# Kernel optimization log

Hardware: AMD Instinct MI355X
Metric: run time of the kernel (lower is better)

The kernel has to match this reference:

```python
import jax, jax.numpy as jnp
import numpy as np

N = 50000
E = 800000
IN_C, HID_C, OUT_C = 128, 128, 64


def setup_inputs() -> dict:
    key = jax.random.key(0)
    k1, k2, k3, k4 = jax.random.split(key, 4)
    x = jax.random.normal(k1, (N, IN_C), dtype=jnp.float32)
    edge_index = jax.random.randint(k2, (2, E), 0, N, dtype=jnp.int32)
    # Glorot-ish init for the two linear layers (PyG GCNConv uses glorot)
    W1 = jax.random.normal(k3, (IN_C, HID_C), dtype=jnp.float32) / np.sqrt(IN_C)
    b1 = jnp.zeros((HID_C,), dtype=jnp.float32)
    W2 = jax.random.normal(k4, (HID_C, OUT_C), dtype=jnp.float32) / np.sqrt(HID_C)
    b2 = jnp.zeros((OUT_C,), dtype=jnp.float32)
    return {"x": x, "edge_index": edge_index, "W1": W1, "b1": b1, "W2": W2, "b2": b2}


def _gcn_norm(edge_index, num_nodes):
    # Add self-loops, then symmetric normalization deg^{-1/2}[row]*deg^{-1/2}[col]
    loop = jnp.arange(num_nodes, dtype=edge_index.dtype)
    row = jnp.concatenate([edge_index[0], loop])  # [E+N] source
    col = jnp.concatenate([edge_index[1], loop])  # [E+N] destination
    deg = jax.ops.segment_sum(jnp.ones_like(col, dtype=jnp.float32), col,
                              num_segments=num_nodes)
    deg_isqrt = jax.lax.rsqrt(deg)  # deg >= 1 due to self-loops
    norm = deg_isqrt[row] * deg_isqrt[col]  # [E+N]
    return row, col, norm


def _gcn_conv(x, row, col, norm, W, b, num_nodes):
    x = x @ W                                   # [N, C_out]
    msg = x[row] * norm[:, None]                # gather + scale, [E+N, C_out]
    out = jax.ops.segment_sum(msg, col, num_segments=num_nodes)  # scatter-add
    return out + b


def reference(x, edge_index, W1, b1, W2, b2):
    num_nodes = x.shape[0]
    row, col, norm = _gcn_norm(edge_index, num_nodes)
    h = _gcn_conv(x, row, col, norm, W1, b1, num_nodes)
    h = jax.nn.relu(h)
    out = _gcn_conv(h, row, col, norm, W2, b2, num_nodes)
    return out
```

## Files before the change

kernel.cpp:

```cpp
#include <hip/hip_runtime.h>


typedef float f32x4 __attribute__((ext_vector_type(4)));
typedef short bf16x8 __attribute__((ext_vector_type(8)));

#define EPB 4096

__device__ inline float bf2f(unsigned short u) {
    return __uint_as_float(((unsigned int)u) << 16);
}
__device__ inline unsigned short f2bf(float f) {
    unsigned int x = __float_as_uint(f);
    x = x + 0x7FFFu + ((x >> 16) & 1u);
    return (unsigned short)(x >> 16);
}
__device__ inline float4 cvt4(ushort4 u) {
    return make_float4(bf2f(u.x), bf2f(u.y), bf2f(u.z), bf2f(u.w));
}
__device__ inline void add4(float4& a, float4 v) {
    a.x += v.x; a.y += v.y; a.z += v.z; a.w += v.w;
}

__global__ __launch_bounds__(256) void k_rhist(const int* __restrict__ col,
                                               int* __restrict__ bbase,
                                               int* __restrict__ bucket_cnt,
                                               const float* __restrict__ W1,
                                               const float* __restrict__ W2,
                                               unsigned short* __restrict__ Wt1,
                                               unsigned short* __restrict__ Wt2,
                                               int e, int nbR, int nbB) {
    if ((int)blockIdx.x >= nbR) {
        int i = ((int)blockIdx.x - nbR) * 256 + threadIdx.x;
        if (i < 16384) {
            int k = i >> 7, nc = i & 127;
            Wt1[nc * 128 + k] = f2bf(W1[i]);
        } else if (i < 24576) {
            int i2 = i - 16384;
            int k = i2 >> 6, nc = i2 & 63;
            Wt2[nc * 128 + k] = f2bf(W2[i2]);
        }
        return;
    }
    __shared__ int h[256];
    int t = threadIdx.x;
    h[t] = 0;
    __syncthreads();
    int base = blockIdx.x * EPB;
#pragma unroll
    for (int i = 0; i < EPB / 256; ++i) {
        int idx = base + t + i * 256;
        if (idx < e) atomicAdd(&h[col[idx] >> 8], 1);
    }
    __syncthreads();
    if (t < nbB) bbase[t * nbR + blockIdx.x] = atomicAdd(&bucket_cnt[t], h[t]);
}

__global__ __launch_bounds__(256) void k_rscatter(const int* __restrict__ row,
                                                  const int* __restrict__ col,
                                                  const int* __restrict__ bucket_cnt,
                                                  const int* __restrict__ bbase,
                                                  unsigned int* __restrict__ tmp,
                                                  int e, int nbR, int nbB) {
    __shared__ int base[256];
    __shared__ int h[256];
    int t = threadIdx.x;
    int v = (t < nbB) ? bucket_cnt[t] : 0;
    base[t] = v;
    __syncthreads();
#pragma unroll
    for (int off = 1; off < 256; off <<= 1) {
        int u = (t >= off) ? base[t - off] : 0;
        __syncthreads();
        base[t] += u;
        __syncthreads();
    }
    int excl = base[t] - v;
    base[t] = excl + ((t < nbB) ? bbase[t * nbR + blockIdx.x] : 0);
    h[t] = 0;
    __syncthreads();
    int b0 = blockIdx.x * EPB;
#pragma unroll
    for (int i = 0; i < EPB / 256; ++i) {
        int idx = b0 + t + i * 256;
        if (idx < e) {
            int c = col[idx];
            int bin = c >> 8;
            int rk = atomicAdd(&h[bin], 1);
            tmp[base[bin] + rk] =
                ((unsigned int)(c & 255) << 16) | (unsigned int)row[idx];
        }
    }
}

__global__ __launch_bounds__(256) void k_bsort(const unsigned int* __restrict__ tmp,
                                               const int* __restrict__ bucket_cnt,
                                               int* __restrict__ indptr,
                                               float* __restrict__ dinv,
                                               unsigned short* __restrict__ srcidx,
                                               int n, int e, int nbB) {
    __shared__ int cnt[256];
    __shared__ int pre[256];
    int b = blockIdx.x;
    int t = threadIdx.x;

    int v = (t < nbB) ? bucket_cnt[t] : 0;
    pre[t] = v;
    __syncthreads();
#pragma unroll
    for (int off = 1; off < 256; off <<= 1) {
        int u = (t >= off) ? pre[t - off] : 0;
        __syncthreads();
        pre[t] += u;
        __syncthreads();
    }
    int beg = pre[b] - ((b < nbB) ? bucket_cnt[b] : 0);
    int end = pre[b];
    __syncthreads();

    cnt[t] = 0;
    __syncthreads();
    for (int i = beg + t; i < end; i += 256) atomicAdd(&cnt[tmp[i] >> 16], 1);
    __syncthreads();
    v = cnt[t];
    pre[t] = v;
    __syncthreads();
#pragma unroll
    for (int off = 1; off < 256; off <<= 1) {
        int u = (t >= off) ? pre[t - off] : 0;
        __syncthreads();
        pre[t] += u;
        __syncthreads();
    }
    int myexcl = pre[t] - v;
    int node = b * 256 + t;
    if (node < n) {
        indptr[node] = beg + myexcl;
        dinv[node] = rsqrtf((float)v + 1.0f);
    }
    if (b == nbB - 1 && t == 0) indptr[n] = e;
    __syncthreads();
    pre[t] = beg + myexcl;
    cnt[t] = 0;
    __syncthreads();
    for (int i = beg + t; i < end; i += 256) {
        unsigned int u = tmp[i];
        int cl = u >> 16;
        int rk = atomicAdd(&cnt[cl], 1);
        srcidx[pre[cl] + rk] = (unsigned short)(u & 0xFFFFu);
    }
}

__global__ __launch_bounds__(256, 2) void k_gemm1(const float* __restrict__ x,
                                                  const unsigned short* __restrict__ Wt,
                                                  const float* __restrict__ dinv,
                                                  unsigned short* __restrict__ hs, int n) {
    __shared__ unsigned short Xs[128 * 136];
    __shared__ unsigned short Ws[128 * 136];
    __shared__ float dinv_s[128];
    int t = threadIdx.x;
    int r0blk = blockIdx.x * 128;

#pragma unroll
    for (int i = 0; i < 8; ++i) {
        int c = t + i * 256;
        int nc = c >> 4;
        int k0 = (c & 15) * 8;
        bf16x8 v = *(const bf16x8*)&Wt[nc * 128 + k0];
        *(bf16x8*)&Ws[nc * 136 + k0] = v;
    }
#pragma unroll
    for (int i = 0; i < 16; ++i) {
        int c = t + i * 256;
        int r = c >> 5;
        int kq = c & 31;
        float4 v = make_float4(0.f, 0.f, 0.f, 0.f);
        int gr = r0blk + r;
        if (gr < n) v = ((const float4*)x)[gr * 32 + kq];
        ushort4 o;
        o.x = f2bf(v.x); o.y = f2bf(v.y); o.z = f2bf(v.z); o.w = f2bf(v.w);
        *(ushort4*)&Xs[r * 136 + kq * 4] = o;
    }
    if (t < 128) {
        int gr = r0blk + t;
        dinv_s[t] = (gr < n) ? dinv[gr] : 0.f;
    }
    __syncthreads();

    int lane = t & 63, wave = t >> 6;
    int lrow = lane & 15;
    int lk = (lane >> 4) * 8;

    f32x4 acc[2][8];
#pragma unroll
    for (int mi = 0; mi < 2; ++mi)
#pragma unroll
        for (int ni = 0; ni < 8; ++ni) acc[mi][ni] = (f32x4){0.f, 0.f, 0.f, 0.f};

#pragma unroll
    for (int ks = 0; ks < 4; ++ks) {
        int kk = ks * 32 + lk;
        bf16x8 a0 = *(bf16x8*)&Xs[(wave * 32 + lrow) * 136 + kk];
        bf16x8 a1 = *(bf16x8*)&Xs[(wave * 32 + 16 + lrow) * 136 + kk];
#pragma unroll
        for (int ni = 0; ni < 8; ++ni) {
            bf16x8 b = *(bf16x8*)&Ws[(ni * 16 + lrow) * 136 + kk];
            acc[0][ni] = __builtin_amdgcn_mfma_f32_16x16x32_bf16(a0, b, acc[0][ni], 0, 0, 0);
            acc[1][ni] = __builtin_amdgcn_mfma_f32_16x16x32_bf16(a1, b, acc[1][ni], 0, 0, 0);
        }
    }

    int rq = (lane >> 4) * 4;
#pragma unroll
    for (int mi = 0; mi < 2; ++mi)
#pragma unroll
        for (int r = 0; r < 4; ++r) {
            int lrw = wave * 32 + mi * 16 + rq + r;
            int grow = r0blk + lrw;
            if (grow < n) {
                float dv = dinv_s[lrw];
#pragma unroll
                for (int ni = 0; ni < 8; ++ni)
                    hs[grow * 128 + ni * 16 + lrow] = f2bf(acc[mi][ni][r] * dv);
            }
        }
}

__global__ __launch_bounds__(256) void k_gather1(const int* __restrict__ indptr,
                                                 const unsigned short* __restrict__ srcidx,
                                                 const unsigned short* __restrict__ hs,
                                                 const float* __restrict__ dinv,
                                                 const float* __restrict__ b1,
                                                 unsigned short* __restrict__ h1, int n) {
    int wid = (blockIdx.x * 256 + threadIdx.x) >> 6;
    if (wid >= n) return;
    int lane = threadIdx.x & 63;
    int half = lane >> 5;
    int hl = lane & 31;
    const ushort4* hv = (const ushort4*)hs;

    int beg = indptr[wid], end = indptr[wid + 1];
    int c0 = (end - beg + 1) >> 1;
    int j    = beg + half * c0;
    int jend = half ? end : (beg + c0);

    float4 a0 = make_float4(0.f, 0.f, 0.f, 0.f), a1 = a0, a2 = a0, a3 = a0;

    for (; j + 7 < jend; j += 8) {
        int s0 = srcidx[j],     s1 = srcidx[j + 1];
        int s2 = srcidx[j + 2], s3 = srcidx[j + 3];
        int s4 = srcidx[j + 4], s5 = srcidx[j + 5];
        int s6 = srcidx[j + 6], s7 = srcidx[j + 7];
        float4 v0 = cvt4(hv[s0 * 32 + hl]);
        float4 v1 = cvt4(hv[s1 * 32 + hl]);
        float4 v2 = cvt4(hv[s2 * 32 + hl]);
        float4 v3 = cvt4(hv[s3 * 32 + hl]);
        float4 v4 = cvt4(hv[s4 * 32 + hl]);
        float4 v5 = cvt4(hv[s5 * 32 + hl]);
        float4 v6 = cvt4(hv[s6 * 32 + hl]);
        float4 v7 = cvt4(hv[s7 * 32 + hl]);
        add4(a0, v0); add4(a1, v1); add4(a2, v2); add4(a3, v3);
        add4(a0, v4); add4(a1, v5); add4(a2, v6); add4(a3, v7);
    }
    if (j + 3 < jend) {
        int s0 = srcidx[j], s1 = srcidx[j + 1], s2 = srcidx[j + 2], s3 = srcidx[j + 3];
        add4(a0, cvt4(hv[s0 * 32 + hl]));
        add4(a1, cvt4(hv[s1 * 32 + hl]));
        add4(a2, cvt4(hv[s2 * 32 + hl]));
        add4(a3, cvt4(hv[s3 * 32 + hl]));
        j += 4;
    }
    for (; j < jend; ++j) add4(a0, cvt4(hv[srcidx[j] * 32 + hl]));

    if (half == 0) add4(a1, cvt4(hv[wid * 32 + hl]));

    float4 tsum;
    tsum.x = a0.x + a1.x + a2.x + a3.x;
    tsum.y = a0.y + a1.y + a2.y + a3.y;
    tsum.z = a0.z + a1.z + a2.z + a3.z;
    tsum.w = a0.w + a1.w + a2.w + a3.w;
    tsum.x += __shfl_xor(tsum.x, 32);
    tsum.y += __shfl_xor(tsum.y, 32);
    tsum.z += __shfl_xor(tsum.z, 32);
    tsum.w += __shfl_xor(tsum.w, 32);

    if (half == 0) {
        float d = dinv[wid];
        float4 bb = *(const float4*)&b1[hl * 4];
        ushort4 o;
        o.x = f2bf(fmaxf(tsum.x * d + bb.x, 0.f));
        o.y = f2bf(fmaxf(tsum.y * d + bb.y, 0.f));
        o.z = f2bf(fmaxf(tsum.z * d + bb.z, 0.f));
        o.w = f2bf(fmaxf(tsum.w * d + bb.w, 0.f));
        ((ushort4*)h1)[wid * 32 + hl] = o;
    }
}

__global__ __launch_bounds__(256, 3) void k_gemm2(const unsigned short* __restrict__ h1,
                                                  const unsigned short* __restrict__ Wt,
                                                  const float* __restrict__ dinv,
                                                  unsigned short* __restrict__ ps2, int n) {
    __shared__ unsigned short Xs[128 * 136];
    __shared__ unsigned short Ws[64 * 136];
    __shared__ float dinv_s[128];
    int t = threadIdx.x;
    int r0blk = blockIdx.x * 128;

#pragma unroll
    for (int i = 0; i < 4; ++i) {
        int c = t + i * 256;
        int nc = c >> 4;
        int k0 = (c & 15) * 8;
        bf16x8 v = *(const bf16x8*)&Wt[nc * 128 + k0];
        *(bf16x8*)&Ws[nc * 136 + k0] = v;
    }
#pragma unroll
    for (int i = 0; i < 8; ++i) {
        int c = t + i * 256;
        int r = c >> 4;
        int k0 = (c & 15) * 8;
        int gr = r0blk + r;
        bf16x8 v = (bf16x8)(short)0;
        if (gr < n) v = *(const bf16x8*)&h1[gr * 128 + k0];
        *(bf16x8*)&Xs[r * 136 + k0] = v;
    }
    if (t < 128) {
        int gr = r0blk + t;
        dinv_s[t] = (gr < n) ? dinv[gr] : 0.f;
    }
    __syncthreads();

    int lane = t & 63, wave = t >> 6;
    int lrow = lane & 15;
    int lk = (lane >> 4) * 8;

    f32x4 acc[2][4];
#pragma unroll
    for (int mi = 0; mi < 2; ++mi)
#pragma unroll
        for (int ni = 0; ni < 4; ++ni) acc[mi][ni] = (f32x4){0.f, 0.f, 0.f, 0.f};

#pragma unroll
    for (int ks = 0; ks < 4; ++ks) {
        int kk = ks * 32 + lk;
        bf16x8 a0 = *(bf16x8*)&Xs[(wave * 32 + lrow) * 136 + kk];
        bf16x8 a1 = *(bf16x8*)&Xs[(wave * 32 + 16 + lrow) * 136 + kk];
#pragma unroll
        for (int ni = 0; ni < 4; ++ni) {
            bf16x8 b = *(bf16x8*)&Ws[(ni * 16 + lrow) * 136 + kk];
            acc[0][ni] = __builtin_amdgcn_mfma_f32_16x16x32_bf16(a0, b, acc[0][ni], 0, 0, 0);
            acc[1][ni] = __builtin_amdgcn_mfma_f32_16x16x32_bf16(a1, b, acc[1][ni], 0, 0, 0);
        }
    }

    int rq = (lane >> 4) * 4;
#pragma unroll
    for (int mi = 0; mi < 2; ++mi)
#pragma unroll
        for (int r = 0; r < 4; ++r) {
            int lrw = wave * 32 + mi * 16 + rq + r;
            int grow = r0blk + lrw;
            if (grow < n) {
                float dv = dinv_s[lrw];
#pragma unroll
                for (int ni = 0; ni < 4; ++ni)
                    ps2[grow * 64 + ni * 16 + lrow] = f2bf(acc[mi][ni][r] * dv);
            }
        }
}

__global__ __launch_bounds__(256) void k_gather2(const int* __restrict__ indptr,
                                                 const unsigned short* __restrict__ srcidx,
                                                 const unsigned short* __restrict__ ps2,
                                                 const float* __restrict__ dinv,
                                                 const float* __restrict__ b2,
                                                 float* __restrict__ out, int n) {
    int wid = (blockIdx.x * 256 + threadIdx.x) >> 6;
    if (wid >= n) return;
    int lane = threadIdx.x & 63;
    int half = lane >> 5;
    int hl = lane & 31;
    const unsigned int* pv = (const unsigned int*)ps2;

    int beg = indptr[wid], end = indptr[wid + 1];
    int c0 = (end - beg + 1) >> 1;
    int j    = beg + half * c0;
    int jend = half ? end : (beg + c0);

    float2 a0 = make_float2(0.f, 0.f), a1 = a0, a2 = a0, a3 = a0;

    for (; j + 7 < jend; j += 8) {
        int s0 = srcidx[j],     s1 = srcidx[j + 1];
        int s2 = srcidx[j + 2], s3 = srcidx[j + 3];
        int s4 = srcidx[j + 4], s5 = srcidx[j + 5];
        int s6 = srcidx[j + 6], s7 = srcidx[j + 7];
        unsigned int u0 = pv[s0 * 32 + hl];
        unsigned int u1 = pv[s1 * 32 + hl];
        unsigned int u2 = pv[s2 * 32 + hl];
        unsigned int u3 = pv[s3 * 32 + hl];
        unsigned int u4 = pv[s4 * 32 + hl];
        unsigned int u5 = pv[s5 * 32 + hl];
        unsigned int u6 = pv[s6 * 32 + hl];
        unsigned int u7 = pv[s7 * 32 + hl];
        a0.x += bf2f((unsigned short)u0); a0.y += bf2f((unsigned short)(u0 >> 16));
        a1.x += bf2f((unsigned short)u1); a1.y += bf2f((unsigned short)(u1 >> 16));
        a2.x += bf2f((unsigned short)u2); a2.y += bf2f((unsigned short)(u2 >> 16));
        a3.x += bf2f((unsigned short)u3); a3.y += bf2f((unsigned short)(u3 >> 16));
        a0.x += bf2f((unsigned short)u4); a0.y += bf2f((unsigned short)(u4 >> 16));
        a1.x += bf2f((unsigned short)u5); a1.y += bf2f((unsigned short)(u5 >> 16));
        a2.x += bf2f((unsigned short)u6); a2.y += bf2f((unsigned short)(u6 >> 16));
        a3.x += bf2f((unsigned short)u7); a3.y += bf2f((unsigned short)(u7 >> 16));
    }
    if (j + 3 < jend) {
        int s0 = srcidx[j], s1 = srcidx[j + 1], s2 = srcidx[j + 2], s3 = srcidx[j + 3];
        unsigned int u0 = pv[s0 * 32 + hl];
        unsigned int u1 = pv[s1 * 32 + hl];
        unsigned int u2 = pv[s2 * 32 + hl];
        unsigned int u3 = pv[s3 * 32 + hl];
        a0.x += bf2f((unsigned short)u0); a0.y += bf2f((unsigned short)(u0 >> 16));
        a1.x += bf2f((unsigned short)u1); a1.y += bf2f((unsigned short)(u1 >> 16));
        a2.x += bf2f((unsigned short)u2); a2.y += bf2f((unsigned short)(u2 >> 16));
        a3.x += bf2f((unsigned short)u3); a3.y += bf2f((unsigned short)(u3 >> 16));
        j += 4;
    }
    for (; j < jend; ++j) {
        unsigned int u = pv[srcidx[j] * 32 + hl];
        a0.x += bf2f((unsigned short)u); a0.y += bf2f((unsigned short)(u >> 16));
    }

    if (half == 0) {
        unsigned int u = pv[wid * 32 + hl];
        a1.x += bf2f((unsigned short)u); a1.y += bf2f((unsigned short)(u >> 16));
    }

    float2 tsum;
    tsum.x = a0.x + a1.x + a2.x + a3.x;
    tsum.y = a0.y + a1.y + a2.y + a3.y;
    tsum.x += __shfl_xor(tsum.x, 32);
    tsum.y += __shfl_xor(tsum.y, 32);

    if (half == 0) {
        float d = dinv[wid];
        float2 bb = *(const float2*)&b2[hl * 2];
        float2 o;
        o.x = tsum.x * d + bb.x;
        o.y = tsum.y * d + bb.y;
        ((float2*)out)[wid * 32 + hl] = o;
    }
}

extern "C" void kernel_launch(void* const* d_in, const int* in_sizes, int n_in,
                              void* d_out, int out_size, void* d_ws, size_t ws_size,
                              hipStream_t stream) {
    const float* x  = (const float*)d_in[0];
    const int*   ei = (const int*)d_in[1];
    const float* W1 = (const float*)d_in[2];
    const float* b1 = (const float*)d_in[3];
    const float* W2 = (const float*)d_in[4];
    const float* b2 = (const float*)d_in[5];
    float* out = (float*)d_out;

    int n = in_sizes[0] / 128;
    int e = in_sizes[1] / 2;
    const int* row = ei;
    const int* col = ei + e;

    int nbR = (e + EPB - 1) / EPB;
    int nbB = (n + 255) / 256;
    int m   = nbB * nbR;

    int* iw = (int*)d_ws;
    size_t o = 0;
    int* bucket_cnt  = iw + o; o += 256;
    int* bbase       = iw + o; o += (size_t)m;           o = (o + 3) & ~(size_t)3;
    int* indptr      = iw + o; o += (size_t)(n + 1);     o = (o + 3) & ~(size_t)3;
    float* dinv      = (float*)(iw + o); o += (size_t)n; o = (o + 3) & ~(size_t)3;
    unsigned int* tmp = (unsigned int*)(iw + o); o += (size_t)e; o = (o + 3) & ~(size_t)3;
    unsigned short* srcidx = (unsigned short*)(iw + o); o += (size_t)(e / 2 + 2); o = (o + 3) & ~(size_t)3;
    unsigned short* Wt1 = (unsigned short*)(iw + o); o += 8192;
    unsigned short* Wt2 = (unsigned short*)(iw + o); o += 4096;
    unsigned short* hs  = (unsigned short*)(iw + o);
    unsigned short* h1  = hs + (size_t)n * 128;
    unsigned short* ps2 = hs;

    hipMemsetAsync(bucket_cnt, 0, 256 * sizeof(int), stream);
    k_rhist<<<nbR + 96, 256, 0, stream>>>(col, bbase, bucket_cnt, W1, W2, Wt1, Wt2, e, nbR, nbB);
    k_rscatter<<<nbR, 256, 0, stream>>>(row, col, bucket_cnt, bbase, tmp, e, nbR, nbB);
    k_bsort<<<nbB, 256, 0, stream>>>(tmp, bucket_cnt, indptr, dinv, srcidx, n, e, nbB);

    int nbg = (n + 127) / 128;
    k_gemm1<<<nbg, 256, 0, stream>>>(x, Wt1, dinv, hs, n);
    k_gather1<<<(n * 64 + 255) / 256, 256, 0, stream>>>(indptr, srcidx, hs, dinv, b1, h1, n);
    k_gemm2<<<nbg, 256, 0, stream>>>(h1, Wt2, dinv, ps2, n);
    k_gather2<<<(n * 64 + 255) / 256, 256, 0, stream>>>(indptr, srcidx, ps2, dinv, b2, out, n);
}
```

Measured before the change: 136.4 us.

## Fuse first GEMM into radix-scatter kernel and move source degree scaling into gather

Removes the dependency of the first GEMM on dinv by dropping the per-row source normalization from its epilogue and applying dinv[src] per edge inside gather1 instead. With that dependency gone, the GEMM blocks are launched in the same grid as the edge-scatter kernel, so both run concurrently and one launch is saved. The cost is an extra random dinv load per edge in gather1, plus the scatter blocks now carry the GEMM's large shared-memory footprint, which lowers their occupancy.

```diff
diff --git a/kernel.cpp b/kernel.cpp
--- a/kernel.cpp
+++ b/kernel.cpp
@@ -17,8 +17,8 @@
 __device__ inline float4 cvt4(ushort4 u) {
     return make_float4(bf2f(u.x), bf2f(u.y), bf2f(u.z), bf2f(u.w));
 }
-__device__ inline void add4(float4& a, float4 v) {
-    a.x += v.x; a.y += v.y; a.z += v.z; a.w += v.w;
+__device__ inline void fma4(float4& a, float4 v, float d) {
+    a.x += v.x * d; a.y += v.y * d; a.z += v.z * d; a.w += v.w * d;
 }
 
 __global__ __launch_bounds__(256) void k_rhist(const int* __restrict__ col,
@@ -55,41 +55,111 @@
     if (t < nbB) bbase[t * nbR + blockIdx.x] = atomicAdd(&bucket_cnt[t], h[t]);
 }
 
-__global__ __launch_bounds__(256) void k_rscatter(const int* __restrict__ row,
+__global__ __launch_bounds__(256, 2) void k_fused(const int* __restrict__ row,
                                                   const int* __restrict__ col,
                                                   const int* __restrict__ bucket_cnt,
                                                   const int* __restrict__ bbase,
                                                   unsigned int* __restrict__ tmp,
-                                                  int e, int nbR, int nbB) {
-    __shared__ int base[256];
-    __shared__ int h[256];
+                                                  const float* __restrict__ x,
+                                                  const unsigned short* __restrict__ Wt,
+                                                  unsigned short* __restrict__ hs,
+                                                  int e, int n, int nbR, int nbB) {
+    __shared__ int sbase[256];
+    __shared__ int sh[256];
+    __shared__ unsigned short Xs[128 * 136];
+    __shared__ unsigned short Ws[128 * 136];
     int t = threadIdx.x;
-    int v = (t < nbB) ? bucket_cnt[t] : 0;
-    base[t] = v;
-    __syncthreads();
-#pragma unroll
-    for (int off = 1; off < 256; off <<= 1) {
-        int u = (t >= off) ? base[t - off] : 0;
-        __syncthreads();
-        base[t] += u;
-        __syncthreads();
-    }
-    int excl = base[t] - v;
-    base[t] = excl + ((t < nbB) ? bbase[t * nbR + blockIdx.x] : 0);
-    h[t] = 0;
-    __syncthreads();
-    int b0 = blockIdx.x * EPB;
-#pragma unroll
-    for (int i = 0; i < EPB / 256; ++i) {
-        int idx = b0 + t + i * 256;
-        if (idx < e) {
-            int c = col[idx];
-            int bin = c >> 8;
-            int rk = atomicAdd(&h[bin], 1);
-            tmp[base[bin] + rk] =
-                ((unsigned int)(c & 255) << 16) | (unsigned int)row[idx];
-        }
-    }
+
+    if ((int)blockIdx.x < nbR) {
+        int v = (t < nbB) ? bucket_cnt[t] : 0;
+        sbase[t] = v;
+        __syncthreads();
+#pragma unroll
+        for (int off = 1; off < 256; off <<= 1) {
+            int u = (t >= off) ? sbase[t - off] : 0;
+            __syncthreads();
+            sbase[t] += u;
+            __syncthreads();
+        }
+        int excl = sbase[t] - v;
+        sbase[t] = excl + ((t < nbB) ? bbase[t * nbR + blockIdx.x] : 0);
+        sh[t] = 0;
+        __syncthreads();
+        int b0 = blockIdx.x * EPB;
+#pragma unroll
+        for (int i = 0; i < EPB / 256; ++i) {
+            int idx = b0 + t + i * 256;
+            if (idx < e) {
+                int c = col[idx];
+                int bin = c >> 8;
+                int rk = atomicAdd(&sh[bin], 1);
+                tmp[sbase[bin] + rk] =
+                    ((unsigned int)(c & 255) << 16) | (unsigned int)row[idx];
+            }
+        }
+        return;
+    }
+
+    int r0blk = ((int)blockIdx.x - nbR) * 128;
+
+#pragma unroll
+    for (int i = 0; i < 8; ++i) {
+        int c = t + i * 256;
+        int nc = c >> 4;
+        int k0 = (c & 15) * 8;
+        bf16x8 v = *(const bf16x8*)&Wt[nc * 128 + k0];
+        *(bf16x8*)&Ws[nc * 136 + k0] = v;
+    }
+#pragma unroll
+    for (int i = 0; i < 16; ++i) {
+        int c = t + i * 256;
+        int r = c >> 5;
+        int kq = c & 31;
+        float4 v = make_float4(0.f, 0.f, 0.f, 0.f);
+        int gr = r0blk + r;
+        if (gr < n) v = ((const float4*)x)[gr * 32 + kq];
+        ushort4 o;
+        o.x = f2bf(v.x); o.y = f2bf(v.y); o.z = f2bf(v.z); o.w = f2bf(v.w);
+        *(ushort4*)&Xs[r * 136 + kq * 4] = o;
+    }
+    __syncthreads();
+
+    int lane = t & 63, wave = t >> 6;
+    int lrow = lane & 15;
+    int lk = (lane >> 4) * 8;
+
+    f32x4 acc[2][8];
+#pragma unroll
+    for (int mi = 0; mi < 2; ++mi)
+#pragma unroll
+        for (int ni = 0; ni < 8; ++ni) acc[mi][ni] = (f32x4){0.f, 0.f, 0.f, 0.f};
+
+#pragma unroll
+    for (int ks = 0; ks < 4; ++ks) {
+        int kk = ks * 32 + lk;
+        bf16x8 a0 = *(bf16x8*)&Xs[(wave * 32 + lrow) * 136 + kk];
+        bf16x8 a1 = *(bf16x8*)&Xs[(wave * 32 + 16 + lrow) * 136 + kk];
+#pragma unroll
+        for (int ni = 0; ni < 8; ++ni) {
+            bf16x8 b = *(bf16x8*)&Ws[(ni * 16 + lrow) * 136 + kk];
+            acc[0][ni] = __builtin_amdgcn_mfma_f32_16x16x32_bf16(a0, b, acc[0][ni], 0, 0, 0);
+            acc[1][ni] = __builtin_amdgcn_mfma_f32_16x16x32_bf16(a1, b, acc[1][ni], 0, 0, 0);
+        }
+    }
+
+    int rq = (lane >> 4) * 4;
+#pragma unroll
+    for (int mi = 0; mi < 2; ++mi)
+#pragma unroll
+        for (int r = 0; r < 4; ++r) {
+            int lrw = wave * 32 + mi * 16 + rq + r;
+            int grow = r0blk + lrw;
+            if (grow < n) {
+#pragma unroll
+                for (int ni = 0; ni < 8; ++ni)
+                    hs[grow * 128 + ni * 16 + lrow] = f2bf(acc[mi][ni][r]);
+            }
+        }
 }
 
 __global__ __launch_bounds__(256) void k_bsort(const unsigned int* __restrict__ tmp,
@@ -148,81 +218,6 @@
         int rk = atomicAdd(&cnt[cl], 1);
         srcidx[pre[cl] + rk] = (unsigned short)(u & 0xFFFFu);
     }
-}
-
-__global__ __launch_bounds__(256, 2) void k_gemm1(const float* __restrict__ x,
-                                                  const unsigned short* __restrict__ Wt,
-                                                  const float* __restrict__ dinv,
-                                                  unsigned short* __restrict__ hs, int n) {
-    __shared__ unsigned short Xs[128 * 136];
-    __shared__ unsigned short Ws[128 * 136];
-    __shared__ float dinv_s[128];
-    int t = threadIdx.x;
-    int r0blk = blockIdx.x * 128;
-
-#pragma unroll
-    for (int i = 0; i < 8; ++i) {
-        int c = t + i * 256;
-        int nc = c >> 4;
-        int k0 = (c & 15) * 8;
-        bf16x8 v = *(const bf16x8*)&Wt[nc * 128 + k0];
-        *(bf16x8*)&Ws[nc * 136 + k0] = v;
-    }
-#pragma unroll
-    for (int i = 0; i < 16; ++i) {
-        int c = t + i * 256;
-        int r = c >> 5;
-        int kq = c & 31;
-        float4 v = make_float4(0.f, 0.f, 0.f, 0.f);
-        int gr = r0blk + r;
-        if (gr < n) v = ((const float4*)x)[gr * 32 + kq];
-        ushort4 o;
-        o.x = f2bf(v.x); o.y = f2bf(v.y); o.z = f2bf(v.z); o.w = f2bf(v.w);
-        *(ushort4*)&Xs[r * 136 + kq * 4] = o;
-    }
-    if (t < 128) {
-        int gr = r0blk + t;
-        dinv_s[t] = (gr < n) ? dinv[gr] : 0.f;
-    }
-    __syncthreads();
-
-    int lane = t & 63, wave = t >> 6;
-    int lrow = lane & 15;
-    int lk = (lane >> 4) * 8;
-
-    f32x4 acc[2][8];
-#pragma unroll
-    for (int mi = 0; mi < 2; ++mi)
-#pragma unroll
-        for (int ni = 0; ni < 8; ++ni) acc[mi][ni] = (f32x4){0.f, 0.f, 0.f, 0.f};
-
-#pragma unroll
-    for (int ks = 0; ks < 4; ++ks) {
-        int kk = ks * 32 + lk;
-        bf16x8 a0 = *(bf16x8*)&Xs[(wave * 32 + lrow) * 136 + kk];
-        bf16x8 a1 = *(bf16x8*)&Xs[(wave * 32 + 16 + lrow) * 136 + kk];
-#pragma unroll
-        for (int ni = 0; ni < 8; ++ni) {
-            bf16x8 b = *(bf16x8*)&Ws[(ni * 16 + lrow) * 136 + kk];
-            acc[0][ni] = __builtin_amdgcn_mfma_f32_16x16x32_bf16(a0, b, acc[0][ni], 0, 0, 0);
-            acc[1][ni] = __builtin_amdgcn_mfma_f32_16x16x32_bf16(a1, b, acc[1][ni], 0, 0, 0);
-        }
-    }
-
-    int rq = (lane >> 4) * 4;
-#pragma unroll
-    for (int mi = 0; mi < 2; ++mi)
-#pragma unroll
-        for (int r = 0; r < 4; ++r) {
-            int lrw = wave * 32 + mi * 16 + rq + r;
-            int grow = r0blk + lrw;
-            if (grow < n) {
-                float dv = dinv_s[lrw];
-#pragma unroll
-                for (int ni = 0; ni < 8; ++ni)
-                    hs[grow * 128 + ni * 16 + lrow] = f2bf(acc[mi][ni][r] * dv);
-            }
-        }
 }
 
 __global__ __launch_bounds__(256) void k_gather1(const int* __restrict__ indptr,
@@ -250,6 +245,8 @@
         int s2 = srcidx[j + 2], s3 = srcidx[j + 3];
         int s4 = srcidx[j + 4], s5 = srcidx[j + 5];
         int s6 = srcidx[j + 6], s7 = srcidx[j + 7];
+        float d0 = dinv[s0], d1 = dinv[s1], d2 = dinv[s2], d3 = dinv[s3];
+        float d4 = dinv[s4], d5 = dinv[s5], d6 = dinv[s6], d7 = dinv[s7];
         float4 v0 = cvt4(hv[s0 * 32 + hl]);
         float4 v1 = cvt4(hv[s1 * 32 + hl]);
         float4 v2 = cvt4(hv[s2 * 32 + hl]);
@@ -258,20 +255,24 @@
         float4 v5 = cvt4(hv[s5 * 32 + hl]);
         float4 v6 = cvt4(hv[s6 * 32 + hl]);
         float4 v7 = cvt4(hv[s7 * 32 + hl]);
-        add4(a0, v0); add4(a1, v1); add4(a2, v2); add4(a3, v3);
-        add4(a0, v4); add4(a1, v5); add4(a2, v6); add4(a3, v7);
+        fma4(a0, v0, d0); fma4(a1, v1, d1); fma4(a2, v2, d2); fma4(a3, v3, d3);
+        fma4(a0, v4, d4); fma4(a1, v5, d5); fma4(a2, v6, d6); fma4(a3, v7, d7);
     }
     if (j + 3 < jend) {
         int s0 = srcidx[j], s1 = srcidx[j + 1], s2 = srcidx[j + 2], s3 = srcidx[j + 3];
-        add4(a0, cvt4(hv[s0 * 32 + hl]));
-        add4(a1, cvt4(hv[s1 * 32 + hl]));
-        add4(a2, cvt4(hv[s2 * 32 + hl]));
-        add4(a3, cvt4(hv[s3 * 32 + hl]));
+        fma4(a0, cvt4(hv[s0 * 32 + hl]), dinv[s0]);
+        fma4(a1, cvt4(hv[s1 * 32 + hl]), dinv[s1]);
+        fma4(a2, cvt4(hv[s2 * 32 + hl]), dinv[s2]);
+        fma4(a3, cvt4(hv[s3 * 32 + hl]), dinv[s3]);
         j += 4;
     }
-    for (; j < jend; ++j) add4(a0, cvt4(hv[srcidx[j] * 32 + hl]));
-
-    if (half == 0) add4(a1, cvt4(hv[wid * 32 + hl]));
+    for (; j < jend; ++j) {
+        int s0 = srcidx[j];
+        fma4(a0, cvt4(hv[s0 * 32 + hl]), dinv[s0]);
+    }
+
+    float dw = dinv[wid];
+    if (half == 0) fma4(a1, cvt4(hv[wid * 32 + hl]), dw);
 
     float4 tsum;
     tsum.x = a0.x + a1.x + a2.x + a3.x;
@@ -284,13 +285,12 @@
     tsum.w += __shfl_xor(tsum.w, 32);
 
     if (half == 0) {
-        float d = dinv[wid];
         float4 bb = *(const float4*)&b1[hl * 4];
         ushort4 o;
-        o.x = f2bf(fmaxf(tsum.x * d + bb.x, 0.f));
-        o.y = f2bf(fmaxf(tsum.y * d + bb.y, 0.f));
-        o.z = f2bf(fmaxf(tsum.z * d + bb.z, 0.f));
-        o.w = f2bf(fmaxf(tsum.w * d + bb.w, 0.f));
+        o.x = f2bf(fmaxf(tsum.x * dw + bb.x, 0.f));
+        o.y = f2bf(fmaxf(tsum.y * dw + bb.y, 0.f));
+        o.z = f2bf(fmaxf(tsum.z * dw + bb.z, 0.f));
+        o.w = f2bf(fmaxf(tsum.w * dw + bb.w, 0.f));
         ((ushort4*)h1)[wid * 32 + hl] = o;
     }
 }
@@ -467,6 +467,7 @@
     int nbR = (e + EPB - 1) / EPB;
     int nbB = (n + 255) / 256;
     int m   = nbB * nbR;
+    int nbg = (n + 127) / 128;
 
     int* iw = (int*)d_ws;
     size_t o = 0;
@@ -484,11 +485,9 @@
 
     hipMemsetAsync(bucket_cnt, 0, 256 * sizeof(int), stream);
     k_rhist<<<nbR + 96, 256, 0, stream>>>(col, bbase, bucket_cnt, W1, W2, Wt1, Wt2, e, nbR, nbB);
-    k_rscatter<<<nbR, 256, 0, stream>>>(row, col, bucket_cnt, bbase, tmp, e, nbR, nbB);
+    k_fused<<<nbR + nbg, 256, 0, stream>>>(row, col, bucket_cnt, bbase, tmp, x, Wt1, hs, e, n, nbR, nbB);
     k_bsort<<<nbB, 256, 0, stream>>>(tmp, bucket_cnt, indptr, dinv, srcidx, n, e, nbB);
 
-    int nbg = (n + 127) / 128;
-    k_gemm1<<<nbg, 256, 0, stream>>>(x, Wt1, dinv, hs, n);
     k_gather1<<<(n * 64 + 255) / 256, 256, 0, stream>>>(indptr, srcidx, hs, dinv, b1, h1, n);
     k_gemm2<<<nbg, 256, 0, stream>>>(h1, Wt2, dinv, ps2, n);
     k_gather2<<<(n * 64 + 255) / 256, 256, 0, stream>>>(indptr, srcidx, ps2, dinv, b2, out, n);
```

After: 131.0 us (median of 2 runs). 1.04x faster.

## Compute degrees in histogram pass and fuse edge scatter with first GEMM

Applied to the files above, without the earlier changes.

The histogram kernel now also accumulates per-node in-degree with global atomics, so dinv no longer depends on the bucket sort. With that dependency gone, the edge scatter and the first feature GEMM are merged into one launch whose blocks split by index, letting the memory-bound scatter overlap the MFMA GEMM and removing one kernel boundary. The cost is 800k extra global atomics on the degree array and a larger memset. The fused kernel also carries the GEMM's large shared-memory footprint into the scatter blocks, which may limit how many of them run at once.

```diff
diff --git a/kernel.cpp b/kernel.cpp
--- a/kernel.cpp
+++ b/kernel.cpp
@@ -24,6 +24,7 @@
 __global__ __launch_bounds__(256) void k_rhist(const int* __restrict__ col,
                                                int* __restrict__ bbase,
                                                int* __restrict__ bucket_cnt,
+                                               int* __restrict__ deg,
                                                const float* __restrict__ W1,
                                                const float* __restrict__ W2,
                                                unsigned short* __restrict__ Wt1,
@@ -49,116 +50,65 @@
 #pragma unroll
     for (int i = 0; i < EPB / 256; ++i) {
         int idx = base + t + i * 256;
-        if (idx < e) atomicAdd(&h[col[idx] >> 8], 1);
+        if (idx < e) {
+            int c = col[idx];
+            atomicAdd(&h[c >> 8], 1);
+            atomicAdd(&deg[c], 1);
+        }
     }
     __syncthreads();
     if (t < nbB) bbase[t * nbR + blockIdx.x] = atomicAdd(&bucket_cnt[t], h[t]);
 }
 
-__global__ __launch_bounds__(256) void k_rscatter(const int* __restrict__ row,
+__global__ __launch_bounds__(256, 2) void k_fused(const int* __restrict__ row,
                                                   const int* __restrict__ col,
                                                   const int* __restrict__ bucket_cnt,
                                                   const int* __restrict__ bbase,
                                                   unsigned int* __restrict__ tmp,
-                                                  int e, int nbR, int nbB) {
-    __shared__ int base[256];
-    __shared__ int h[256];
-    int t = threadIdx.x;
-    int v = (t < nbB) ? bucket_cnt[t] : 0;
-    base[t] = v;
-    __syncthreads();
-#pragma unroll
-    for (int off = 1; off < 256; off <<= 1) {
-        int u = (t >= off) ? base[t - off] : 0;
-        __syncthreads();
-        base[t] += u;
-        __syncthreads();
-    }
-    int excl = base[t] - v;
-    base[t] = excl + ((t < nbB) ? bbase[t * nbR + blockIdx.x] : 0);
-    h[t] = 0;
-    __syncthreads();
-    int b0 = blockIdx.x * EPB;
-#pragma unroll
-    for (int i = 0; i < EPB / 256; ++i) {
-        int idx = b0 + t + i * 256;
-        if (idx < e) {
-            int c = col[idx];
-            int bin = c >> 8;
-            int rk = atomicAdd(&h[bin], 1);
-            tmp[base[bin] + rk] =
-                ((unsigned int)(c & 255) << 16) | (unsigned int)row[idx];
-        }
-    }
-}
-
-__global__ __launch_bounds__(256) void k_bsort(const unsigned int* __restrict__ tmp,
-                                               const int* __restrict__ bucket_cnt,
-                                               int* __restrict__ indptr,
-                                               float* __restrict__ dinv,
-                                               unsigned short* __restrict__ srcidx,
-                                               int n, int e, int nbB) {
-    __shared__ int cnt[256];
-    __shared__ int pre[256];
-    int b = blockIdx.x;
-    int t = threadIdx.x;
-
-    int v = (t < nbB) ? bucket_cnt[t] : 0;
-    pre[t] = v;
-    __syncthreads();
-#pragma unroll
-    for (int off = 1; off < 256; off <<= 1) {
-        int u = (t >= off) ? pre[t - off] : 0;
-        __syncthreads();
-        pre[t] += u;
-        __syncthreads();
-    }
-    int beg = pre[b] - ((b < nbB) ? bucket_cnt[b] : 0);
-    int end = pre[b];
-    __syncthreads();
-
-    cnt[t] = 0;
-    __syncthreads();
-    for (int i = beg + t; i < end; i += 256) atomicAdd(&cnt[tmp[i] >> 16], 1);
-    __syncthreads();
-    v = cnt[t];
-    pre[t] = v;
-    __syncthreads();
-#pragma unroll
-    for (int off = 1; off < 256; off <<= 1) {
-        int u = (t >= off) ? pre[t - off] : 0;
-        __syncthreads();
-        pre[t] += u;
-        __syncthreads();
-    }
-    int myexcl = pre[t] - v;
-    int node = b * 256 + t;
-    if (node < n) {
-        indptr[node] = beg + myexcl;
-        dinv[node] = rsqrtf((float)v + 1.0f);
-    }
-    if (b == nbB - 1 && t == 0) indptr[n] = e;
-    __syncthreads();
-    pre[t] = beg + myexcl;
-    cnt[t] = 0;
-    __syncthreads();
-    for (int i = beg + t; i < end; i += 256) {
-        unsigned int u = tmp[i];
-        int cl = u >> 16;
-        int rk = atomicAdd(&cnt[cl], 1);
-        srcidx[pre[cl] + rk] = (unsigned short)(u & 0xFFFFu);
-    }
-}
-
-__global__ __launch_bounds__(256, 2) void k_gemm1(const float* __restrict__ x,
+                                                  const float* __restrict__ x,
                                                   const unsigned short* __restrict__ Wt,
-                                                  const float* __restrict__ dinv,
-                                                  unsigned short* __restrict__ hs, int n) {
+                                                  const int* __restrict__ deg,
+                                                  float* __restrict__ dinv,
+                                                  unsigned short* __restrict__ hs,
+                                                  int e, int n, int nbR, int nbB) {
+    __shared__ int sbase[256];
+    __shared__ int sh[256];
     __shared__ unsigned short Xs[128 * 136];
     __shared__ unsigned short Ws[128 * 136];
     __shared__ float dinv_s[128];
     int t = threadIdx.x;
-    int r0blk = blockIdx.x * 128;
+
+    if ((int)blockIdx.x < nbR) {
+        int v = (t < nbB) ? bucket_cnt[t] : 0;
+        sbase[t] = v;
+        __syncthreads();
+#pragma unroll
+        for (int off = 1; off < 256; off <<= 1) {
+            int u = (t >= off) ? sbase[t - off] : 0;
+            __syncthreads();
+            sbase[t] += u;
+            __syncthreads();
+        }
+        int excl = sbase[t] - v;
+        sbase[t] = excl + ((t < nbB) ? bbase[t * nbR + blockIdx.x] : 0);
+        sh[t] = 0;
+        __syncthreads();
+        int b0 = blockIdx.x * EPB;
+#pragma unroll
+        for (int i = 0; i < EPB / 256; ++i) {
+            int idx = b0 + t + i * 256;
+            if (idx < e) {
+                int c = col[idx];
+                int bin = c >> 8;
+                int rk = atomicAdd(&sh[bin], 1);
+                tmp[sbase[bin] + rk] =
+                    ((unsigned int)(c & 255) << 16) | (unsigned int)row[idx];
+            }
+        }
+        return;
+    }
+
+    int r0blk = ((int)blockIdx.x - nbR) * 128;
 
 #pragma unroll
     for (int i = 0; i < 8; ++i) {
@@ -182,7 +132,12 @@
     }
     if (t < 128) {
         int gr = r0blk + t;
-        dinv_s[t] = (gr < n) ? dinv[gr] : 0.f;
+        float dv = 0.f;
+        if (gr < n) {
+            dv = rsqrtf((float)deg[gr] + 1.0f);
+            dinv[gr] = dv;
+        }
+        dinv_s[t] = dv;
     }
     __syncthreads();
 
@@ -223,6 +178,60 @@
                     hs[grow * 128 + ni * 16 + lrow] = f2bf(acc[mi][ni][r] * dv);
             }
         }
+}
+
+__global__ __launch_bounds__(256) void k_bsort(const unsigned int* __restrict__ tmp,
+                                               const int* __restrict__ bucket_cnt,
+                                               int* __restrict__ indptr,
+                                               unsigned short* __restrict__ srcidx,
+                                               int n, int e, int nbB) {
+    __shared__ int cnt[256];
+    __shared__ int pre[256];
+    int b = blockIdx.x;
+    int t = threadIdx.x;
+
+    int v = (t < nbB) ? bucket_cnt[t] : 0;
+    pre[t] = v;
+    __syncthreads();
+#pragma unroll
+    for (int off = 1; off < 256; off <<= 1) {
+        int u = (t >= off) ? pre[t - off] : 0;
+        __syncthreads();
+        pre[t] += u;
+        __syncthreads();
+    }
+    int beg = pre[b] - ((b < nbB) ? bucket_cnt[b] : 0);
+    int end = pre[b];
+    __syncthreads();
+
+    cnt[t] = 0;
+    __syncthreads();
+    for (int i = beg + t; i < end; i += 256) atomicAdd(&cnt[tmp[i] >> 16], 1);
+    __syncthreads();
+    v = cnt[t];
+    pre[t] = v;
+    __syncthreads();
+#pragma unroll
+    for (int off = 1; off < 256; off <<= 1) {
+        int u = (t >= off) ? pre[t - off] : 0;
+        __syncthreads();
+        pre[t] += u;
+        __syncthreads();
+    }
+    int myexcl = pre[t] - v;
+    int node = b * 256 + t;
+    if (node < n) indptr[node] = beg + myexcl;
+    if (b == nbB - 1 && t == 0) indptr[n] = e;
+    __syncthreads();
+    pre[t] = beg + myexcl;
+    cnt[t] = 0;
+    __syncthreads();
+    for (int i = beg + t; i < end; i += 256) {
+        unsigned int u = tmp[i];
+        int cl = u >> 16;
+        int rk = atomicAdd(&cnt[cl], 1);
+        srcidx[pre[cl] + rk] = (unsigned short)(u & 0xFFFFu);
+    }
 }
 
 __global__ __launch_bounds__(256) void k_gather1(const int* __restrict__ indptr,
@@ -467,10 +476,12 @@
     int nbR = (e + EPB - 1) / EPB;
     int nbB = (n + 255) / 256;
     int m   = nbB * nbR;
+    int nbg = (n + 127) / 128;
 
     int* iw = (int*)d_ws;
     size_t o = 0;
     int* bucket_cnt  = iw + o; o += 256;
+    int* deg         = iw + o; o += (size_t)n;           o = (o + 3) & ~(size_t)3;
     int* bbase       = iw + o; o += (size_t)m;           o = (o + 3) & ~(size_t)3;
     int* indptr      = iw + o; o += (size_t)(n + 1);     o = (o + 3) & ~(size_t)3;
     float* dinv      = (float*)(iw + o); o += (size_t)n; o = (o + 3) & ~(size_t)3;
@@ -482,13 +493,11 @@
     unsigned short* h1  = hs + (size_t)n * 128;
     unsigned short* ps2 = hs;
 
-    hipMemsetAsync(bucket_cnt, 0, 256 * sizeof(int), stream);
-    k_rhist<<<nbR + 96, 256, 0, stream>>>(col, bbase, bucket_cnt, W1, W2, Wt1, Wt2, e, nbR, nbB);
-    k_rscatter<<<nbR, 256, 0, stream>>>(row, col, bucket_cnt, bbase, tmp, e, nbR, nbB);
-    k_bsort<<<nbB, 256, 0, stream>>>(tmp, bucket_cnt, indptr, dinv, srcidx, n, e, nbB);
-
-    int nbg = (n + 127) / 128;
-    k_gemm1<<<nbg, 256, 0, stream>>>(x, Wt1, dinv, hs, n);
+    hipMemsetAsync(bucket_cnt, 0, (256 + (size_t)n) * sizeof(int), stream);
+    k_rhist<<<nbR + 96, 256, 0, stream>>>(col, bbase, bucket_cnt, deg, W1, W2, Wt1, Wt2, e, nbR, nbB);
+    k_fused<<<nbR + nbg, 256, 0, stream>>>(row, col, bucket_cnt, bbase, tmp, x, Wt1, deg, dinv, hs, e, n, nbR, nbB);
+    k_bsort<<<nbB, 256, 0, stream>>>(tmp, bucket_cnt, indptr, srcidx, n, e, nbB);
+
     k_gather1<<<(n * 64 + 255) / 256, 256, 0, stream>>>(indptr, srcidx, hs, dinv, b1, h1, n);
     k_gemm2<<<nbg, 256, 0, stream>>>(h1, Wt2, dinv, ps2, n);
     k_gather2<<<(n * 64 + 255) / 256, 256, 0, stream>>>(indptr, srcidx, ps2, dinv, b2, out, n);
```

New measurement: 159.2 us. 16.7% more time.
